# Optimization experiments

Measured on AMD Instinct MI355X. Metric: run time of the kernel, lower is better.

The kernel has to match this reference:

```python
import jax, jax.numpy as jnp
import numpy as np

B, S, D = 4, 2048, 1024
H = 16
DH = D // H
MLP_DIM = 4096
EPS = 1e-6


def setup_inputs() -> dict:
    key = jax.random.key(0)
    ks = jax.random.split(key, 16)
    sd = lambda fi, fo: (1.0 / np.sqrt(fi))
    return {
        "x": jax.random.normal(ks[0], (B, S, D), jnp.float32),
        "Wq": jax.random.normal(ks[1], (D, D), jnp.float32) * sd(D, D),
        "bq": jnp.zeros((D,), jnp.float32),
        "Wk": jax.random.normal(ks[2], (D, D), jnp.float32) * sd(D, D),
        "bk": jnp.zeros((D,), jnp.float32),
        "Wv": jax.random.normal(ks[3], (D, D), jnp.float32) * sd(D, D),
        "bv": jnp.zeros((D,), jnp.float32),
        "Wo": jax.random.normal(ks[4], (D, D), jnp.float32) * sd(D, D),
        "bo": jnp.zeros((D,), jnp.float32),
        "ln1_g": jnp.ones((D,), jnp.float32),
        "ln1_b": jnp.zeros((D,), jnp.float32),
        "ln2_g": jnp.ones((D,), jnp.float32),
        "ln2_b": jnp.zeros((D,), jnp.float32),
        "W1": jax.random.normal(ks[5], (D, MLP_DIM), jnp.float32) * sd(D, MLP_DIM),
        "b1": jax.random.normal(ks[6], (MLP_DIM,), jnp.float32) * 1e-6,
        "W2": jax.random.normal(ks[7], (MLP_DIM, D), jnp.float32) * sd(MLP_DIM, D),
        "b2": jax.random.normal(ks[8], (D,), jnp.float32) * 1e-6,
    }


def _layernorm(x, g, b):
    mu = jnp.mean(x, axis=-1, keepdims=True)
    var = jnp.mean(jnp.square(x - mu), axis=-1, keepdims=True)
    return (x - mu) * jax.lax.rsqrt(var + EPS) * g + b


def reference(x, Wq, bq, Wk, bk, Wv, bv, Wo, bo,
              ln1_g, ln1_b, ln2_g, ln2_b, W1, b1, W2, b2):
    h = x
    xn = _layernorm(x, ln1_g, ln1_b)
    # Q/K/V: [B,S,D] -> [B,H,S,DH]
    def split_heads(t):
        return t.reshape(B, S, H, DH).transpose(0, 2, 1, 3)
    Q = split_heads(xn @ Wq + bq)
    K = split_heads(xn @ Wk + bk)
    V = split_heads(xn @ Wv + bv)
    scores = jnp.einsum("bhqd,bhkd->bhqk", Q, K) / np.sqrt(DH).astype(np.float32)
    a = jax.nn.softmax(scores, axis=-1)
    r = jnp.einsum("bhqk,bhkd->bhqd", a, V)          # [B,H,S,DH]
    r = r.transpose(0, 2, 1, 3).reshape(B, S, D)      # merge heads
    r = r @ Wo + bo
    x = r + h
    h = x
    xn = _layernorm(x, ln2_g, ln2_b)
    m = jax.nn.gelu(xn @ W1 + b1, approximate=False)
    m = m @ W2 + b2
    return m + h
```

## Files before the change

kernel.cpp:

```cpp
#include <hip/hip_runtime.h>
#include <math.h>

#define B_ 4
#define S_ 2048
#define D_ 1024
#define H_ 16
#define MLP_ 4096
#define MROWS 8192

typedef __attribute__((ext_vector_type(4))) float f32x4;
typedef __attribute__((ext_vector_type(16))) float f32x16;
typedef __attribute__((ext_vector_type(8))) __bf16 bf16x8;
typedef __attribute__((ext_vector_type(4))) __bf16 bf16x4;
typedef __attribute__((ext_vector_type(8))) unsigned short us8;
typedef unsigned short u16;
typedef unsigned int u32;

__device__ __forceinline__ void gload16(const void* g, void* l) {
    __builtin_amdgcn_global_load_lds((const __attribute__((address_space(1))) u32*)g,
                                     (__attribute__((address_space(3))) u32*)l, 16, 0, 0);
}

__device__ __forceinline__ float gelu_f(float v) {
    return 0.5f * v * (1.0f + erff(v * 0.70710678118654752f));
}

__global__ __launch_bounds__(256) void ln_bf16_k(const float* __restrict__ x,
                                                 const float* __restrict__ g,
                                                 const float* __restrict__ b,
                                                 u16* __restrict__ y) {
    int row = blockIdx.x;
    int tid = threadIdx.x;
    const float* xr = x + (size_t)row * D_;
    f32x4 v = *(const f32x4*)(xr + tid * 4);
    float s = v.x + v.y + v.z + v.w;
    float ss = v.x * v.x + v.y * v.y + v.z * v.z + v.w * v.w;
    for (int off = 32; off > 0; off >>= 1) {
        s += __shfl_down(s, off, 64);
        ss += __shfl_down(ss, off, 64);
    }
    __shared__ float rs[4], rss[4];
    int lane = tid & 63, wid = tid >> 6;
    if (lane == 0) { rs[wid] = s; rss[wid] = ss; }
    __syncthreads();
    s = rs[0] + rs[1] + rs[2] + rs[3];
    ss = rss[0] + rss[1] + rss[2] + rss[3];
    float mu = s * (1.0f / D_);
    float var = ss * (1.0f / D_) - mu * mu;
    float inv = rsqrtf(var + 1e-6f);
    f32x4 gg = *(const f32x4*)(g + tid * 4);
    f32x4 bb = *(const f32x4*)(b + tid * 4);
    bf16x4 o = {(__bf16)((v.x - mu) * inv * gg.x + bb.x),
                (__bf16)((v.y - mu) * inv * gg.y + bb.y),
                (__bf16)((v.z - mu) * inv * gg.z + bb.z),
                (__bf16)((v.w - mu) * inv * gg.w + bb.w)};
    *(bf16x4*)(y + (size_t)row * D_ + tid * 4) = o;
}

__global__ void pack3_k(const float* __restrict__ a, const float* __restrict__ b,
                        const float* __restrict__ c, float* __restrict__ o) {
    const float* s = blockIdx.x == 0 ? a : (blockIdx.x == 1 ? b : c);
    o[blockIdx.x * 1024 + threadIdx.x] = s[threadIdx.x];
}

__global__ __launch_bounds__(256) void wtrans_k(const float* __restrict__ W,
                                                u16* __restrict__ Wt, int K, int N) {
    __shared__ float T[32][33];
    int tid = threadIdx.x;
    int k0 = blockIdx.y * 32, n0 = blockIdx.x * 32;
    int r = tid >> 3, c4 = (tid & 7) * 4;
    f32x4 v = *(const f32x4*)&W[(size_t)(k0 + r) * N + n0 + c4];
    T[r][c4 + 0] = v.x; T[r][c4 + 1] = v.y; T[r][c4 + 2] = v.z; T[r][c4 + 3] = v.w;
    __syncthreads();
    int n = tid >> 3, kk = (tid & 7) * 4;
    bf16x4 o = {(__bf16)T[kk + 0][n], (__bf16)T[kk + 1][n],
                (__bf16)T[kk + 2][n], (__bf16)T[kk + 3][n]};
    *(bf16x4*)&Wt[(size_t)(n0 + n) * K + k0 + kk] = o;
}

__device__ __forceinline__ int sigma_perm(int s) {
    return (s & 48) | (s & 3) | (((s >> 2) & 1) << 3) | (((s >> 3) & 1) << 2);
}
__global__ __launch_bounds__(256) void vtrans_k(const u16* __restrict__ QKV,
                                                u16* __restrict__ Vt) {
    __shared__ u16 T[64][80];
    int tid = threadIdx.x;
    int s0 = blockIdx.x * 64;
    int bh = blockIdx.y, b = bh >> 4, h = bh & 15;
    int r = tid >> 2, c0 = (tid & 3) * 16;
    const u16* src = QKV + (size_t)(b * S_ + s0 + r) * 3072 + 2048 + h * 64 + c0;
    us8 v0 = *(const us8*)src;
    us8 v1 = *(const us8*)(src + 8);
    *(us8*)&T[r][c0] = v0;
    *(us8*)&T[r][c0 + 8] = v1;
    __syncthreads();
    int dh = tid >> 2, s8 = (tid & 3) * 16;
    us8 o0, o1;
#pragma unroll
    for (int i = 0; i < 8; ++i) {
        o0[i] = T[sigma_perm(s8 + i)][dh];
        o1[i] = T[sigma_perm(s8 + 8 + i)][dh];
    }
    u16* dst = Vt + (size_t)(bh * 64 + dh) * S_ + s0 + s8;
    *(us8*)dst = o0;
    *(us8*)(dst + 8) = o1;
}

template <int EPI>
__global__ __launch_bounds__(256) void gemm_bf16(const u16* __restrict__ A,
                                                 const u16* __restrict__ Wt,
                                                 const float* __restrict__ bias,
                                                 const float* __restrict__ res,
                                                 void* __restrict__ Cout,
                                                 int M, int N, int K) {
    __shared__ u16 As[3][128 * 32];
    __shared__ u16 Bs[3][128 * 32];
    const int tid = threadIdx.x;
    const int lane = tid & 63;
    const int w = tid >> 6;
    const int nwg = gridDim.x * gridDim.y;
    int hw = blockIdx.x + gridDim.x * blockIdx.y;
    int lg = (hw & 7) * (nwg >> 3) + (hw >> 3);
    const int row0 = (lg / gridDim.x) * 128;
    const int col0 = (lg % gridDim.x) * 128;
    const int l15 = lane & 15, l16 = lane >> 4;
    const int wr = w >> 1, wc = w & 1;

    f32x4 acc[4][4];
#pragma unroll
    for (int i = 0; i < 4; ++i)
#pragma unroll
        for (int j = 0; j < 4; ++j) acc[i][j] = (f32x4){0.f, 0.f, 0.f, 0.f};

    const int srow = w * 32 + (lane >> 2);
    const size_t sboff = (size_t)(lane & 3) * 16;
    const char* Ag = (const char*)A + ((size_t)(row0 + srow) * K) * 2 + sboff;
    const char* Bg = (const char*)Wt + ((size_t)(col0 + srow) * K) * 2 + sboff;
    const size_t rstep = (size_t)16 * K * 2;
    const int woff = w * 2048;
    const int T = K >> 5;

#define STAGE(t, bi) do {                                      \
        size_t kb = (size_t)(t) << 6;                          \
        char* asw = (char*)As + (bi) * 8192 + woff;            \
        char* bsw = (char*)Bs + (bi) * 8192 + woff;            \
        gload16(Ag + kb, asw);                                 \
        gload16(Ag + kb + rstep, asw + 1024);                  \
        gload16(Bg + kb, bsw);                                 \
        gload16(Bg + kb + rstep, bsw + 1024);                  \
    } while (0)

    STAGE(0, 0);
    STAGE(1, 1);
    asm volatile("s_waitcnt vmcnt(4)" ::: "memory");
    __builtin_amdgcn_s_barrier();
    __builtin_amdgcn_sched_barrier(0);

    int bi = 0;
    for (int t = 0; t < T; ++t) {
        if (t + 2 < T) {
            int nb = bi + 2; if (nb >= 3) nb -= 3;
            STAGE(t + 2, nb);
        }
        const char* Ab = (const char*)As + bi * 8192;
        const char* Bb = (const char*)Bs + bi * 8192;
        bf16x8 af[4], bfr[4];
#pragma unroll
        for (int f = 0; f < 4; ++f) {
            af[f] = *(const bf16x8*)(Ab + (size_t)(wr * 64 + f * 16 + l15) * 64 + (l16 << 4));
            bfr[f] = *(const bf16x8*)(Bb + (size_t)(wc * 64 + f * 16 + l15) * 64 + (l16 << 4));
        }
        __builtin_amdgcn_s_setprio(1);
#pragma unroll
        for (int fi = 0; fi < 4; ++fi)
#pragma unroll
            for (int fj = 0; fj < 4; ++fj)
                acc[fi][fj] = __builtin_amdgcn_mfma_f32_16x16x32_bf16(af[fi], bfr[fj], acc[fi][fj], 0, 0, 0);
        __builtin_amdgcn_s_setprio(0);
        if (t + 2 < T) {
            asm volatile("s_waitcnt vmcnt(4)" ::: "memory");
        } else {
            asm volatile("s_waitcnt vmcnt(0)" ::: "memory");
        }
        __builtin_amdgcn_s_barrier();
        __builtin_amdgcn_sched_barrier(0);
        if (++bi >= 3) bi = 0;
    }
#undef STAGE

    const int rb = row0 + wr * 64 + (l16 << 2);
    const int cb = col0 + wc * 64 + l15;
#pragma unroll
    for (int fi = 0; fi < 4; ++fi)
#pragma unroll
        for (int fj = 0; fj < 4; ++fj) {
            int c = cb + fj * 16;
            float bv = bias[c];
#pragma unroll
            for (int rr = 0; rr < 4; ++rr) {
                int r = rb + fi * 16 + rr;
                float v = acc[fi][fj][rr] + bv;
                if (EPI == 1) v = gelu_f(v);
                if (EPI == 2) {
                    v += res[(size_t)r * N + c];
                    ((float*)Cout)[(size_t)r * N + c] = v;
                } else {
                    ((__bf16*)Cout)[(size_t)r * N + c] = (__bf16)v;
                }
            }
        }
}

__global__ __launch_bounds__(256) void attn_mfma(const u16* __restrict__ QKV,
                                                 const u16* __restrict__ Vt,
                                                 u16* __restrict__ O) {
    __shared__ u16 Ks[2][64 * 64];
    __shared__ u16 Vs[2][64 * 64];
    const int tid = threadIdx.x, lane = tid & 63, w = tid >> 6;
    int hw = blockIdx.x + gridDim.x * blockIdx.y;
    int lg = (hw & 7) * 128 + (hw >> 3);
    const int bh = lg >> 4, b = bh >> 4, h = bh & 15;
    const int q0 = (lg & 15) * 128;
    const int l31 = lane & 31, lh = lane >> 5;

    const u16* Qp = QKV + (size_t)(b * S_ + q0 + w * 32 + l31) * 3072 + h * 64 + lh * 8;
    bf16x8 qf[4];
    qf[0] = *(const bf16x8*)(Qp);
    qf[1] = *(const bf16x8*)(Qp + 16);
    qf[2] = *(const bf16x8*)(Qp + 32);
    qf[3] = *(const bf16x8*)(Qp + 48);

    f32x16 oacc[2];
#pragma unroll
    for (int i = 0; i < 16; ++i) { oacc[0][i] = 0.f; oacc[1][i] = 0.f; }
    float mold = -1e30f, lsum = 0.f;

    const int sr = lane >> 3;
    const size_t soff = (size_t)(((lane & 7) ^ sr) << 4);
    const char* Kg = (const char*)QKV + ((size_t)b * S_ * 3072 + 1024 + h * 64) * 2;
    const char* Vg = (const char*)Vt + (size_t)bh * 64 * S_ * 2;
    const float C2 = 0.18033688011112f;
    const float THRRAW = 44.0f;

    const char* kp0 = Kg + (size_t)(w * 16 + sr) * 6144 + soff;
    const char* kp1 = kp0 + 8 * 6144;
    const char* vp0 = Vg + (size_t)(w * 16 + sr) * 4096 + soff;
    const char* vp1 = vp0 + 8 * 4096;
    const size_t KADV = 64 * 6144;
    const size_t VADV = 128;
    char* ksA = (char*)Ks[0] + w * 2048;
    char* ksB = (char*)Ks[1] + w * 2048;
    char* vsA = (char*)Vs[0] + w * 2048;
    char* vsB = (char*)Vs[1] + w * 2048;

    gload16(kp0, ksA); gload16(kp1, ksA + 1024);
    gload16(vp0, vsA); gload16(vp1, vsA + 1024);
    kp0 += KADV; kp1 += KADV; vp0 += VADV; vp1 += VADV;
    __syncthreads();

    for (int kt = 0; kt < S_ / 64; ++kt) {
        const int cur = kt & 1;
        if (kt < S_ / 64 - 1) {
            char* kd = cur ? ksA : ksB;
            char* vd = cur ? vsA : vsB;
            gload16(kp0, kd); gload16(kp1, kd + 1024);
            gload16(vp0, vd); gload16(vp1, vd + 1024);
            kp0 += KADV; kp1 += KADV; vp0 += VADV; vp1 += VADV;
        }

        const char* Kb_ = (const char*)Ks[cur];
        f32x16 sfr[2];
        __builtin_amdgcn_s_setprio(1);
#pragma unroll
        for (int kh = 0; kh < 2; ++kh) {
            int r = kh * 32 + l31;
            int rsw = (r & 7) << 4;
            const char* Kr = Kb_ + r * 128;
            f32x16 t;
#pragma unroll
            for (int i = 0; i < 16; ++i) t[i] = 0.f;
#pragma unroll
            for (int ds = 0; ds < 4; ++ds) {
                bf16x8 kf = *(const bf16x8*)(Kr + ((((ds * 2 + lh) << 4)) ^ rsw));
                t = __builtin_amdgcn_mfma_f32_32x32x16_bf16(kf, qf[ds], t, 0, 0, 0);
            }
            sfr[kh] = t;
        }
        __builtin_amdgcn_s_setprio(0);

        float mx = fmaxf(sfr[0][0], sfr[1][0]);
#pragma unroll
        for (int i = 1; i < 16; ++i) mx = fmaxf(mx, fmaxf(sfr[0][i], sfr[1][i]));
        mx = fmaxf(mx, __shfl_xor(mx, 32, 64));

        bool need = mx > mold + THRRAW;
        if (__any(need)) {
            float mnew = fmaxf(mold, mx);
            float al = __builtin_amdgcn_exp2f((mold - mnew) * C2);
            lsum *= al;
            mold = mnew;
#pragma unroll
            for (int i = 0; i < 16; ++i) { oacc[0][i] *= al; oacc[1][i] *= al; }
        }

        float nm = -mold * C2;
        float pv0[16], pv1[16];
        float psum = 0.f;
#pragma unroll
        for (int i = 0; i < 16; ++i) {
            pv0[i] = __builtin_amdgcn_exp2f(fmaf(sfr[0][i], C2, nm));
            pv1[i] = __builtin_amdgcn_exp2f(fmaf(sfr[1][i], C2, nm));
            psum += pv0[i] + pv1[i];
        }
        psum += __shfl_xor(psum, 32, 64);
        lsum += psum;

        bf16x8 pf[4];
#pragma unroll
        for (int j = 0; j < 8; ++j) {
            pf[0][j] = (__bf16)pv0[j];
            pf[1][j] = (__bf16)pv0[8 + j];
            pf[2][j] = (__bf16)pv1[j];
            pf[3][j] = (__bf16)pv1[8 + j];
        }

        {
            const char* Vb_ = (const char*)Vs[cur];
            __builtin_amdgcn_s_setprio(1);
#pragma unroll
            for (int dh = 0; dh < 2; ++dh) {
                int r = dh * 32 + l31;
                int rsw = (r & 7) << 4;
                const char* Vr = Vb_ + r * 128;
#pragma unroll
                for (int ks = 0; ks < 4; ++ks) {
                    bf16x8 vf = *(const bf16x8*)(Vr + ((((ks * 2 + lh) << 4)) ^ rsw));
                    oacc[dh] = __builtin_amdgcn_mfma_f32_32x32x16_bf16(vf, pf[ks], oacc[dh], 0, 0, 0);
                }
            }
            __builtin_amdgcn_s_setprio(0);
        }
        __syncthreads();
    }

    float invl = 1.0f / lsum;
    char* Og = (char*)O + ((size_t)(b * S_ + q0 + w * 32 + l31) * 1024 + h * 64) * 2;
#pragma unroll
    for (int dh = 0; dh < 2; ++dh)
#pragma unroll
        for (int t4 = 0; t4 < 4; ++t4) {
            int db = dh * 32 + t4 * 8 + lh * 4;
            bf16x4 ov = {(__bf16)(oacc[dh][t4 * 4] * invl),
                         (__bf16)(oacc[dh][t4 * 4 + 1] * invl),
                         (__bf16)(oacc[dh][t4 * 4 + 2] * invl),
                         (__bf16)(oacc[dh][t4 * 4 + 3] * invl)};
            *(bf16x4*)(Og + db * 2) = ov;
        }
}

extern "C" void kernel_launch(void* const* d_in, const int* in_sizes, int n_in,
                              void* d_out, int out_size, void* d_ws, size_t ws_size,
                              hipStream_t stream) {
    const float* x     = (const float*)d_in[0];
    const float* Wq    = (const float*)d_in[1];
    const float* bq    = (const float*)d_in[2];
    const float* Wk    = (const float*)d_in[3];
    const float* bk    = (const float*)d_in[4];
    const float* Wv    = (const float*)d_in[5];
    const float* bv    = (const float*)d_in[6];
    const float* Wo    = (const float*)d_in[7];
    const float* bo    = (const float*)d_in[8];
    const float* ln1_g = (const float*)d_in[9];
    const float* ln1_b = (const float*)d_in[10];
    const float* ln2_g = (const float*)d_in[11];
    const float* ln2_b = (const float*)d_in[12];
    const float* W1    = (const float*)d_in[13];
    const float* b1    = (const float*)d_in[14];
    const float* W2    = (const float*)d_in[15];
    const float* b2    = (const float*)d_in[16];
    float* out = (float*)d_out;

    const size_t MB = 1ull << 20;
    char* ws = (char*)d_ws;
    u16* QKVb = (u16*)(ws + 0 * MB);
    u16* aout = (u16*)(ws + 48 * MB);
    u16* mid  = (u16*)(ws + 0 * MB);
    float* x2 = (float*)(ws + 64 * MB);
    float* bqkv = (float*)(ws + 64 * MB);
    u16* xn   = (u16*)(ws + 96 * MB);
    u16* Vt   = (u16*)(ws + 96 * MB);
    u16* xn2  = (u16*)(ws + 96 * MB);
    u16* Wqkvt = (u16*)(ws + 112 * MB);
    u16* Wot  = Wqkvt + (size_t)3072 * D_;
    u16* W1t  = (u16*)(ws + 112 * MB);
    u16* W2t  = (u16*)(ws + 120 * MB);

    wtrans_k<<<dim3(32, 32), 256, 0, stream>>>(Wq, Wqkvt, D_, D_);
    wtrans_k<<<dim3(32, 32), 256, 0, stream>>>(Wk, Wqkvt + (size_t)D_ * D_, D_, D_);
    wtrans_k<<<dim3(32, 32), 256, 0, stream>>>(Wv, Wqkvt + (size_t)2 * D_ * D_, D_, D_);
    wtrans_k<<<dim3(32, 32), 256, 0, stream>>>(Wo, Wot, D_, D_);
    wtrans_k<<<dim3(32, 128), 256, 0, stream>>>(W2, W2t, MLP_, D_);
    pack3_k<<<3, 1024, 0, stream>>>(bq, bk, bv, bqkv);

    ln_bf16_k<<<MROWS, 256, 0, stream>>>(x, ln1_g, ln1_b, xn);
    gemm_bf16<0><<<dim3(24, 64), 256, 0, stream>>>(xn, Wqkvt, bqkv, nullptr, QKVb, MROWS, 3072, D_);
    vtrans_k<<<dim3(32, 64), 256, 0, stream>>>(QKVb, Vt);
    attn_mfma<<<dim3(16, 64), 256, 0, stream>>>(QKVb, Vt, aout);
    gemm_bf16<2><<<dim3(8, 64), 256, 0, stream>>>(aout, Wot, bo, x, x2, MROWS, D_, D_);
    wtrans_k<<<dim3(128, 32), 256, 0, stream>>>(W1, W1t, D_, MLP_);
    ln_bf16_k<<<MROWS, 256, 0, stream>>>(x2, ln2_g, ln2_b, xn2);
    gemm_bf16<1><<<dim3(32, 64), 256, 0, stream>>>(xn2, W1t, b1, nullptr, mid, MROWS, MLP_, D_);
    gemm_bf16<2><<<dim3(8, 64), 256, 0, stream>>>(mid, W2t, b2, x2, (void*)out, MROWS, D_, MLP_);
}
```

Before: 465.1 us.

## Switch GEMMs to 256x128 tiles with 512 threads, BK=64 and XOR-swizzled LDS

Replaces the 128x128 GEMM with a 256x128 block tile run by 8 waves. The K step per stage doubles to 64, and the LDS layout uses an XOR swizzle on 16-byte chunks to avoid bank conflicts on fragment reads. The aim is more reuse of the B tile per load, fewer barriers per unit of K, and fewer LDS conflicts. In exchange it uses more LDS (about 144KB for three stages), which limits occupancy, and it halves the grid size, which may leave CUs idle on the smaller N=1024 GEMMs.

```diff
diff --git a/kernel.cpp b/kernel.cpp
--- a/kernel.cpp
+++ b/kernel.cpp
@@ -107,21 +107,21 @@
 }
 
 template <int EPI>
-__global__ __launch_bounds__(256) void gemm_bf16(const u16* __restrict__ A,
-                                                 const u16* __restrict__ Wt,
-                                                 const float* __restrict__ bias,
-                                                 const float* __restrict__ res,
-                                                 void* __restrict__ Cout,
-                                                 int M, int N, int K) {
-    __shared__ u16 As[3][128 * 32];
-    __shared__ u16 Bs[3][128 * 32];
+__global__ __launch_bounds__(512) void gemm256(const u16* __restrict__ A,
+                                               const u16* __restrict__ Wt,
+                                               const float* __restrict__ bias,
+                                               const float* __restrict__ res,
+                                               void* __restrict__ Cout,
+                                               int M, int N, int K) {
+    __shared__ u16 AsArr[3 * 16384];
+    __shared__ u16 BsArr[3 * 8192];
     const int tid = threadIdx.x;
     const int lane = tid & 63;
     const int w = tid >> 6;
     const int nwg = gridDim.x * gridDim.y;
     int hw = blockIdx.x + gridDim.x * blockIdx.y;
     int lg = (hw & 7) * (nwg >> 3) + (hw >> 3);
-    const int row0 = (lg / gridDim.x) * 128;
+    const int row0 = (lg / gridDim.x) * 256;
     const int col0 = (lg % gridDim.x) * 128;
     const int l15 = lane & 15, l16 = lane >> 4;
     const int wr = w >> 1, wc = w & 1;
@@ -132,74 +132,82 @@
 #pragma unroll
         for (int j = 0; j < 4; ++j) acc[i][j] = (f32x4){0.f, 0.f, 0.f, 0.f};
 
-    const int srow = w * 32 + (lane >> 2);
-    const size_t sboff = (size_t)(lane & 3) * 16;
-    const char* Ag = (const char*)A + ((size_t)(row0 + srow) * K) * 2 + sboff;
-    const char* Bg = (const char*)Wt + ((size_t)(col0 + srow) * K) * 2 + sboff;
-    const size_t rstep = (size_t)16 * K * 2;
-    const int woff = w * 2048;
-    const int T = K >> 5;
-
-#define STAGE(t, bi) do {                                      \
-        size_t kb = (size_t)(t) << 6;                          \
-        char* asw = (char*)As + (bi) * 8192 + woff;            \
-        char* bsw = (char*)Bs + (bi) * 8192 + woff;            \
-        gload16(Ag + kb, asw);                                 \
-        gload16(Ag + kb + rstep, asw + 1024);                  \
-        gload16(Bg + kb, bsw);                                 \
-        gload16(Bg + kb + rstep, bsw + 1024);                  \
+    const int lr = lane >> 3;
+    const int chunk = (lane & 7) ^ lr;
+    const size_t Kb = (size_t)K * 2;
+    const char* pa0 = (const char*)A + (size_t)(row0 + 0   + 8 * w + lr) * Kb + chunk * 16;
+    const char* pa1 = (const char*)A + (size_t)(row0 + 64  + 8 * w + lr) * Kb + chunk * 16;
+    const char* pa2 = (const char*)A + (size_t)(row0 + 128 + 8 * w + lr) * Kb + chunk * 16;
+    const char* pa3 = (const char*)A + (size_t)(row0 + 192 + 8 * w + lr) * Kb + chunk * 16;
+    const char* pb0 = (const char*)Wt + (size_t)(col0 + 0  + 8 * w + lr) * Kb + chunk * 16;
+    const char* pb1 = (const char*)Wt + (size_t)(col0 + 64 + 8 * w + lr) * Kb + chunk * 16;
+    const int T = K >> 6;
+
+#define STAGE(bufi) do {                                         \
+        char* ad = (char*)AsArr + (bufi) * 32768 + w * 1024;     \
+        char* bd = (char*)BsArr + (bufi) * 16384 + w * 1024;     \
+        gload16(pa0, ad);           gload16(pa1, ad + 8192);     \
+        gload16(pa2, ad + 16384);   gload16(pa3, ad + 24576);    \
+        gload16(pb0, bd);           gload16(pb1, bd + 8192);     \
+        pa0 += 128; pa1 += 128; pa2 += 128; pa3 += 128;          \
+        pb0 += 128; pb1 += 128;                                  \
     } while (0)
 
-    STAGE(0, 0);
-    STAGE(1, 1);
-    asm volatile("s_waitcnt vmcnt(4)" ::: "memory");
+    STAGE(0);
+    STAGE(1);
+    asm volatile("s_waitcnt vmcnt(6)" ::: "memory");
     __builtin_amdgcn_s_barrier();
     __builtin_amdgcn_sched_barrier(0);
 
-    int bi = 0;
+    const int sw = (l15 & 7) << 4;
+    int cur = 0, stg = 2;
     for (int t = 0; t < T; ++t) {
+        if (t + 2 < T) STAGE(stg);
+        const char* Ab = (const char*)AsArr + cur * 32768;
+        const char* Bb = (const char*)BsArr + cur * 16384;
+#pragma unroll
+        for (int h = 0; h < 2; ++h) {
+            const int ko = ((h << 6) | (l16 << 4)) ^ sw;
+            bf16x8 af[4], bfv[4];
+#pragma unroll
+            for (int m = 0; m < 4; ++m)
+                af[m] = *(const bf16x8*)(Ab + (wr * 64 + m * 16 + l15) * 128 + ko);
+#pragma unroll
+            for (int n = 0; n < 4; ++n)
+                bfv[n] = *(const bf16x8*)(Bb + (wc * 64 + n * 16 + l15) * 128 + ko);
+            __builtin_amdgcn_s_setprio(1);
+#pragma unroll
+            for (int m = 0; m < 4; ++m)
+#pragma unroll
+                for (int n = 0; n < 4; ++n)
+                    acc[m][n] = __builtin_amdgcn_mfma_f32_16x16x32_bf16(af[m], bfv[n], acc[m][n], 0, 0, 0);
+            __builtin_amdgcn_s_setprio(0);
+        }
+        if (t == T - 1) break;
         if (t + 2 < T) {
-            int nb = bi + 2; if (nb >= 3) nb -= 3;
-            STAGE(t + 2, nb);
-        }
-        const char* Ab = (const char*)As + bi * 8192;
-        const char* Bb = (const char*)Bs + bi * 8192;
-        bf16x8 af[4], bfr[4];
-#pragma unroll
-        for (int f = 0; f < 4; ++f) {
-            af[f] = *(const bf16x8*)(Ab + (size_t)(wr * 64 + f * 16 + l15) * 64 + (l16 << 4));
-            bfr[f] = *(const bf16x8*)(Bb + (size_t)(wc * 64 + f * 16 + l15) * 64 + (l16 << 4));
-        }
-        __builtin_amdgcn_s_setprio(1);
-#pragma unroll
-        for (int fi = 0; fi < 4; ++fi)
-#pragma unroll
-            for (int fj = 0; fj < 4; ++fj)
-                acc[fi][fj] = __builtin_amdgcn_mfma_f32_16x16x32_bf16(af[fi], bfr[fj], acc[fi][fj], 0, 0, 0);
-        __builtin_amdgcn_s_setprio(0);
-        if (t + 2 < T) {
-            asm volatile("s_waitcnt vmcnt(4)" ::: "memory");
+            asm volatile("s_waitcnt vmcnt(6)" ::: "memory");
         } else {
             asm volatile("s_waitcnt vmcnt(0)" ::: "memory");
         }
         __builtin_amdgcn_s_barrier();
         __builtin_amdgcn_sched_barrier(0);
-        if (++bi >= 3) bi = 0;
+        cur = cur + 1 == 3 ? 0 : cur + 1;
+        stg = stg + 1 == 3 ? 0 : stg + 1;
     }
 #undef STAGE
 
     const int rb = row0 + wr * 64 + (l16 << 2);
     const int cb = col0 + wc * 64 + l15;
 #pragma unroll
-    for (int fi = 0; fi < 4; ++fi)
-#pragma unroll
-        for (int fj = 0; fj < 4; ++fj) {
-            int c = cb + fj * 16;
+    for (int m = 0; m < 4; ++m)
+#pragma unroll
+        for (int n = 0; n < 4; ++n) {
+            int c = cb + n * 16;
             float bv = bias[c];
 #pragma unroll
             for (int rr = 0; rr < 4; ++rr) {
-                int r = rb + fi * 16 + rr;
-                float v = acc[fi][fj][rr] + bv;
+                int r = rb + m * 16 + rr;
+                float v = acc[m][n][rr] + bv;
                 if (EPI == 1) v = gelu_f(v);
                 if (EPI == 2) {
                     v += res[(size_t)r * N + c];
@@ -403,12 +411,12 @@
     pack3_k<<<3, 1024, 0, stream>>>(bq, bk, bv, bqkv);
 
     ln_bf16_k<<<MROWS, 256, 0, stream>>>(x, ln1_g, ln1_b, xn);
-    gemm_bf16<0><<<dim3(24, 64), 256, 0, stream>>>(xn, Wqkvt, bqkv, nullptr, QKVb, MROWS, 3072, D_);
+    gemm256<0><<<dim3(24, 32), 512, 0, stream>>>(xn, Wqkvt, bqkv, nullptr, QKVb, MROWS, 3072, D_);
     vtrans_k<<<dim3(32, 64), 256, 0, stream>>>(QKVb, Vt);
     attn_mfma<<<dim3(16, 64), 256, 0, stream>>>(QKVb, Vt, aout);
-    gemm_bf16<2><<<dim3(8, 64), 256, 0, stream>>>(aout, Wot, bo, x, x2, MROWS, D_, D_);
+    gemm256<2><<<dim3(8, 32), 512, 0, stream>>>(aout, Wot, bo, x, x2, MROWS, D_, D_);
     wtrans_k<<<dim3(128, 32), 256, 0, stream>>>(W1, W1t, D_, MLP_);
     ln_bf16_k<<<MROWS, 256, 0, stream>>>(x2, ln2_g, ln2_b, xn2);
-    gemm_bf16<1><<<dim3(32, 64), 256, 0, stream>>>(xn2, W1t, b1, nullptr, mid, MROWS, MLP_, D_);
-    gemm_bf16<2><<<dim3(8, 64), 256, 0, stream>>>(mid, W2t, b2, x2, (void*)out, MROWS, D_, MLP_);
-}
+    gemm256<1><<<dim3(32, 32), 512, 0, stream>>>(xn2, W1t, b1, nullptr, mid, MROWS, MLP_, D_);
+    gemm256<2><<<dim3(8, 32), 512, 0, stream>>>(mid, W2t, b2, x2, (void*)out, MROWS, D_, MLP_);
+}
```

After: 478.3 us. +2.8%, slower.

## Process two query tiles per wave in attention to reuse K/V fragments

Applied to the files above, without the earlier changes.

Each wave now handles 64 query rows as two 32-row sub-tiles, so every K and V fragment read from LDS feeds two MFMAs. The block tile grows to 256 queries and the grid is halved. The key loop is also split into two 32-key chunks, with softmax and the PV update interleaved per chunk. This cuts LDS traffic and K/V loads per query, at the cost of more registers (doubled accumulators and Q fragments) and fewer blocks, which may lower occupancy.

```diff
diff --git a/kernel.cpp b/kernel.cpp
--- a/kernel.cpp
+++ b/kernel.cpp
@@ -218,22 +218,24 @@
     __shared__ u16 Vs[2][64 * 64];
     const int tid = threadIdx.x, lane = tid & 63, w = tid >> 6;
     int hw = blockIdx.x + gridDim.x * blockIdx.y;
-    int lg = (hw & 7) * 128 + (hw >> 3);
-    const int bh = lg >> 4, b = bh >> 4, h = bh & 15;
-    const int q0 = (lg & 15) * 128;
+    int lg = (hw & 7) * 64 + (hw >> 3);
+    const int bh = lg >> 3, b = bh >> 4, h = bh & 15;
+    const int q0 = (lg & 7) * 256;
     const int l31 = lane & 31, lh = lane >> 5;
 
-    const u16* Qp = QKV + (size_t)(b * S_ + q0 + w * 32 + l31) * 3072 + h * 64 + lh * 8;
-    bf16x8 qf[4];
-    qf[0] = *(const bf16x8*)(Qp);
-    qf[1] = *(const bf16x8*)(Qp + 16);
-    qf[2] = *(const bf16x8*)(Qp + 32);
-    qf[3] = *(const bf16x8*)(Qp + 48);
-
-    f32x16 oacc[2];
-#pragma unroll
-    for (int i = 0; i < 16; ++i) { oacc[0][i] = 0.f; oacc[1][i] = 0.f; }
-    float mold = -1e30f, lsum = 0.f;
+    const u16* Qp0 = QKV + (size_t)(b * S_ + q0 + w * 64 + l31) * 3072 + h * 64 + lh * 8;
+    const u16* Qp1 = Qp0 + (size_t)32 * 3072;
+    bf16x8 qa[4], qb[4];
+#pragma unroll
+    for (int ds = 0; ds < 4; ++ds) {
+        qa[ds] = *(const bf16x8*)(Qp0 + ds * 16);
+        qb[ds] = *(const bf16x8*)(Qp1 + ds * 16);
+    }
+
+    f32x16 oa[2], ob[2];
+#pragma unroll
+    for (int i = 0; i < 16; ++i) { oa[0][i] = 0.f; oa[1][i] = 0.f; ob[0][i] = 0.f; ob[1][i] = 0.f; }
+    float m0 = -1e30f, l0 = 0.f, m1 = -1e30f, l1 = 0.f;
 
     const int sr = lane >> 3;
     const size_t soff = (size_t)(((lane & 7) ^ sr) << 4);
@@ -267,94 +269,118 @@
             gload16(vp0, vd); gload16(vp1, vd + 1024);
             kp0 += KADV; kp1 += KADV; vp0 += VADV; vp1 += VADV;
         }
-
         const char* Kb_ = (const char*)Ks[cur];
-        f32x16 sfr[2];
-        __builtin_amdgcn_s_setprio(1);
-#pragma unroll
-        for (int kh = 0; kh < 2; ++kh) {
-            int r = kh * 32 + l31;
-            int rsw = (r & 7) << 4;
+        const char* Vb_ = (const char*)Vs[cur];
+
+#pragma unroll
+        for (int c = 0; c < 2; ++c) {
+            const int r = c * 32 + l31;
+            const int rsw = (r & 7) << 4;
             const char* Kr = Kb_ + r * 128;
-            f32x16 t;
-#pragma unroll
-            for (int i = 0; i < 16; ++i) t[i] = 0.f;
+            bf16x8 kf[4];
+#pragma unroll
+            for (int ds = 0; ds < 4; ++ds)
+                kf[ds] = *(const bf16x8*)(Kr + ((((ds * 2 + lh) << 4)) ^ rsw));
+            f32x16 t0, t1;
+#pragma unroll
+            for (int i = 0; i < 16; ++i) { t0[i] = 0.f; t1[i] = 0.f; }
+            __builtin_amdgcn_s_setprio(1);
 #pragma unroll
             for (int ds = 0; ds < 4; ++ds) {
-                bf16x8 kf = *(const bf16x8*)(Kr + ((((ds * 2 + lh) << 4)) ^ rsw));
-                t = __builtin_amdgcn_mfma_f32_32x32x16_bf16(kf, qf[ds], t, 0, 0, 0);
-            }
-            sfr[kh] = t;
-        }
-        __builtin_amdgcn_s_setprio(0);
-
-        float mx = fmaxf(sfr[0][0], sfr[1][0]);
-#pragma unroll
-        for (int i = 1; i < 16; ++i) mx = fmaxf(mx, fmaxf(sfr[0][i], sfr[1][i]));
-        mx = fmaxf(mx, __shfl_xor(mx, 32, 64));
-
-        bool need = mx > mold + THRRAW;
-        if (__any(need)) {
-            float mnew = fmaxf(mold, mx);
-            float al = __builtin_amdgcn_exp2f((mold - mnew) * C2);
-            lsum *= al;
-            mold = mnew;
-#pragma unroll
-            for (int i = 0; i < 16; ++i) { oacc[0][i] *= al; oacc[1][i] *= al; }
-        }
-
-        float nm = -mold * C2;
-        float pv0[16], pv1[16];
-        float psum = 0.f;
-#pragma unroll
-        for (int i = 0; i < 16; ++i) {
-            pv0[i] = __builtin_amdgcn_exp2f(fmaf(sfr[0][i], C2, nm));
-            pv1[i] = __builtin_amdgcn_exp2f(fmaf(sfr[1][i], C2, nm));
-            psum += pv0[i] + pv1[i];
-        }
-        psum += __shfl_xor(psum, 32, 64);
-        lsum += psum;
-
-        bf16x8 pf[4];
-#pragma unroll
-        for (int j = 0; j < 8; ++j) {
-            pf[0][j] = (__bf16)pv0[j];
-            pf[1][j] = (__bf16)pv0[8 + j];
-            pf[2][j] = (__bf16)pv1[j];
-            pf[3][j] = (__bf16)pv1[8 + j];
-        }
-
-        {
-            const char* Vb_ = (const char*)Vs[cur];
+                t0 = __builtin_amdgcn_mfma_f32_32x32x16_bf16(kf[ds], qa[ds], t0, 0, 0, 0);
+                t1 = __builtin_amdgcn_mfma_f32_32x32x16_bf16(kf[ds], qb[ds], t1, 0, 0, 0);
+            }
+            __builtin_amdgcn_s_setprio(0);
+
+            float mx0 = fmaxf(t0[0], t0[1]);
+#pragma unroll
+            for (int i = 2; i < 16; ++i) mx0 = fmaxf(mx0, t0[i]);
+            mx0 = fmaxf(mx0, __shfl_xor(mx0, 32, 64));
+            if (__any(mx0 > m0 + THRRAW)) {
+                float mnew = fmaxf(m0, mx0);
+                float al = __builtin_amdgcn_exp2f((m0 - mnew) * C2);
+                l0 *= al; m0 = mnew;
+#pragma unroll
+                for (int i = 0; i < 16; ++i) { oa[0][i] *= al; oa[1][i] *= al; }
+            }
+            float nm0 = -m0 * C2;
+            float p0[16];
+            float ps0 = 0.f;
+#pragma unroll
+            for (int i = 0; i < 16; ++i) {
+                p0[i] = __builtin_amdgcn_exp2f(fmaf(t0[i], C2, nm0));
+                ps0 += p0[i];
+            }
+            ps0 += __shfl_xor(ps0, 32, 64);
+            l0 += ps0;
+
+            float mx1 = fmaxf(t1[0], t1[1]);
+#pragma unroll
+            for (int i = 2; i < 16; ++i) mx1 = fmaxf(mx1, t1[i]);
+            mx1 = fmaxf(mx1, __shfl_xor(mx1, 32, 64));
+            if (__any(mx1 > m1 + THRRAW)) {
+                float mnew = fmaxf(m1, mx1);
+                float al = __builtin_amdgcn_exp2f((m1 - mnew) * C2);
+                l1 *= al; m1 = mnew;
+#pragma unroll
+                for (int i = 0; i < 16; ++i) { ob[0][i] *= al; ob[1][i] *= al; }
+            }
+            float nm1 = -m1 * C2;
+            float p1[16];
+            float ps1 = 0.f;
+#pragma unroll
+            for (int i = 0; i < 16; ++i) {
+                p1[i] = __builtin_amdgcn_exp2f(fmaf(t1[i], C2, nm1));
+                ps1 += p1[i];
+            }
+            ps1 += __shfl_xor(ps1, 32, 64);
+            l1 += ps1;
+
+            bf16x8 pa0, pa1, pb0, pb1;
+#pragma unroll
+            for (int j = 0; j < 8; ++j) {
+                pa0[j] = (__bf16)p0[j];
+                pa1[j] = (__bf16)p0[8 + j];
+                pb0[j] = (__bf16)p1[j];
+                pb1[j] = (__bf16)p1[8 + j];
+            }
+
             __builtin_amdgcn_s_setprio(1);
 #pragma unroll
             for (int dh = 0; dh < 2; ++dh) {
-                int r = dh * 32 + l31;
-                int rsw = (r & 7) << 4;
-                const char* Vr = Vb_ + r * 128;
-#pragma unroll
-                for (int ks = 0; ks < 4; ++ks) {
-                    bf16x8 vf = *(const bf16x8*)(Vr + ((((ks * 2 + lh) << 4)) ^ rsw));
-                    oacc[dh] = __builtin_amdgcn_mfma_f32_32x32x16_bf16(vf, pf[ks], oacc[dh], 0, 0, 0);
-                }
+                const int vr = dh * 32 + l31;
+                const int vrsw = (vr & 7) << 4;
+                const char* Vr = Vb_ + vr * 128;
+                bf16x8 vfa = *(const bf16x8*)(Vr + ((((4 * c + lh) << 4)) ^ vrsw));
+                bf16x8 vfb = *(const bf16x8*)(Vr + ((((4 * c + 2 + lh) << 4)) ^ vrsw));
+                oa[dh] = __builtin_amdgcn_mfma_f32_32x32x16_bf16(vfa, pa0, oa[dh], 0, 0, 0);
+                ob[dh] = __builtin_amdgcn_mfma_f32_32x32x16_bf16(vfa, pb0, ob[dh], 0, 0, 0);
+                oa[dh] = __builtin_amdgcn_mfma_f32_32x32x16_bf16(vfb, pa1, oa[dh], 0, 0, 0);
+                ob[dh] = __builtin_amdgcn_mfma_f32_32x32x16_bf16(vfb, pb1, ob[dh], 0, 0, 0);
             }
             __builtin_amdgcn_s_setprio(0);
         }
         __syncthreads();
     }
 
-    float invl = 1.0f / lsum;
-    char* Og = (char*)O + ((size_t)(b * S_ + q0 + w * 32 + l31) * 1024 + h * 64) * 2;
+    float inv0 = 1.0f / l0, inv1 = 1.0f / l1;
+    char* Og0 = (char*)O + ((size_t)(b * S_ + q0 + w * 64 + l31) * 1024 + h * 64) * 2;
+    char* Og1 = Og0 + (size_t)32 * 2048;
 #pragma unroll
     for (int dh = 0; dh < 2; ++dh)
 #pragma unroll
         for (int t4 = 0; t4 < 4; ++t4) {
             int db = dh * 32 + t4 * 8 + lh * 4;
-            bf16x4 ov = {(__bf16)(oacc[dh][t4 * 4] * invl),
-                         (__bf16)(oacc[dh][t4 * 4 + 1] * invl),
-                         (__bf16)(oacc[dh][t4 * 4 + 2] * invl),
-                         (__bf16)(oacc[dh][t4 * 4 + 3] * invl)};
-            *(bf16x4*)(Og + db * 2) = ov;
+            bf16x4 ov0 = {(__bf16)(oa[dh][t4 * 4] * inv0),
+                          (__bf16)(oa[dh][t4 * 4 + 1] * inv0),
+                          (__bf16)(oa[dh][t4 * 4 + 2] * inv0),
+                          (__bf16)(oa[dh][t4 * 4 + 3] * inv0)};
+            *(bf16x4*)(Og0 + db * 2) = ov0;
+            bf16x4 ov1 = {(__bf16)(ob[dh][t4 * 4] * inv1),
+                          (__bf16)(ob[dh][t4 * 4 + 1] * inv1),
+                          (__bf16)(ob[dh][t4 * 4 + 2] * inv1),
+                          (__bf16)(ob[dh][t4 * 4 + 3] * inv1)};
+            *(bf16x4*)(Og1 + db * 2) = ov1;
         }
 }
 
@@ -405,7 +431,7 @@
     ln_bf16_k<<<MROWS, 256, 0, stream>>>(x, ln1_g, ln1_b, xn);
     gemm_bf16<0><<<dim3(24, 64), 256, 0, stream>>>(xn, Wqkvt, bqkv, nullptr, QKVb, MROWS, 3072, D_);
     vtrans_k<<<dim3(32, 64), 256, 0, stream>>>(QKVb, Vt);
-    attn_mfma<<<dim3(16, 64), 256, 0, stream>>>(QKVb, Vt, aout);
+    attn_mfma<<<dim3(8, 64), 256, 0, stream>>>(QKVb, Vt, aout);
     gemm_bf16<2><<<dim3(8, 64), 256, 0, stream>>>(aout, Wot, bo, x, x2, MROWS, D_, D_);
     wtrans_k<<<dim3(128, 32), 256, 0, stream>>>(W1, W1t, D_, MLP_);
     ln_bf16_k<<<MROWS, 256, 0, stream>>>(x2, ln2_g, ln2_b, xn2);
```

After: 486.9 us. +4.7%, slower.
